# Kernel tuning notes

Measured on AMD Instinct MI355X. Metric: run time of the kernel, lower is better.

## Reference

```python
import jax, jax.numpy as jnp
import numpy as np

B, S, D, H = 8, 1300, 1080, 12
DK = D // H  # 90
FF = 3 * D   # 3240
EPS = 1e-5


def _layernorm(x, g, b):
    m = jnp.mean(x, axis=-1, keepdims=True)
    v = jnp.var(x, axis=-1, keepdims=True)
    return (x - m) * jax.lax.rsqrt(v + EPS) * g + b


def _rotate_half(x):
    x1, x2 = jnp.split(x, 2, axis=-1)
    return jnp.concatenate([-x2, x1], axis=-1)


def _rope(x, cos, sin):
    # x: [B,H,S,DK]; cos/sin: [S,DK] broadcast over batch/heads
    return x * cos + _rotate_half(x) * sin


def setup_inputs() -> dict:
    key = jax.random.key(0)
    ks = jax.random.split(key, 20)
    w = lambda k, sh: jax.random.normal(k, sh, dtype=jnp.float32) * 0.02
    inp = {
        'x': jax.random.normal(ks[0], (B, S, D), dtype=jnp.float32),
        'mask': jnp.tril(jnp.ones((S, S), dtype=jnp.int32))[None, None, :, :],
        'Wq': w(ks[1], (D, D)), 'bq': jnp.zeros((D,), jnp.float32),
        'Wk': w(ks[2], (D, D)), 'bk': jnp.zeros((D,), jnp.float32),
        'Wv': w(ks[3], (D, D)), 'bv': jnp.zeros((D,), jnp.float32),
        'Wo': w(ks[4], (D, D)), 'bo': jnp.zeros((D,), jnp.float32),
        'W1': w(ks[5], (D, FF)), 'b1': jnp.zeros((FF,), jnp.float32),
        'W2': w(ks[6], (FF, D)), 'b2': jnp.zeros((D,), jnp.float32),
        'W3': w(ks[7], (D, FF)), 'b3': jnp.zeros((FF,), jnp.float32),
        'ln1_g': jnp.ones((D,), jnp.float32), 'ln1_b': jnp.zeros((D,), jnp.float32),
        'ln2_g': jnp.ones((D,), jnp.float32), 'ln2_b': jnp.zeros((D,), jnp.float32),
    }
    # RoPE tables (buffers, not trainable)
    inv_freq = 1.0 / (10000.0 ** (jnp.arange(0, DK, 2, dtype=jnp.float32) / DK))
    t = jnp.arange(S, dtype=jnp.float32)
    freqs = t[:, None] * inv_freq[None, :]          # [S, DK/2]
    emb = jnp.concatenate([freqs, freqs], axis=-1)  # [S, DK]
    inp['rope_cos'] = jnp.cos(emb)
    inp['rope_sin'] = jnp.sin(emb)
    return inp


def reference(x, mask, Wq, bq, Wk, bk, Wv, bv, Wo, bo,
              W1, b1, W2, b2, W3, b3, ln1_g, ln1_b, ln2_g, ln2_b,
              rope_cos, rope_sin):
    # pre-norm attention block
    x2 = _layernorm(x, ln1_g, ln1_b)
    q = (x2 @ Wq + bq).reshape(B, S, H, DK).transpose(0, 2, 1, 3)  # [B,H,S,DK]
    k = (x2 @ Wk + bk).reshape(B, S, H, DK).transpose(0, 2, 1, 3)
    v = (x2 @ Wv + bv).reshape(B, S, H, DK).transpose(0, 2, 1, 3)
    q = _rope(q, rope_cos, rope_sin)
    k = _rope(k, rope_cos, rope_sin)
    scores = jnp.einsum('bhqd,bhkd->bhqk', q, k) / jnp.sqrt(jnp.float32(DK))
    scores = jnp.where(mask == 0, jnp.float32(-1e9), scores)
    p = jax.nn.softmax(scores, axis=-1)
    attn = jnp.einsum('bhqk,bhkd->bhqd', p, v)
    attn = attn.transpose(0, 2, 1, 3).reshape(B, S, D)
    x = x + (attn @ Wo + bo)
    # pre-norm SwiGLU FFN block
    x2 = _layernorm(x, ln2_g, ln2_b)
    h = jax.nn.silu(x2 @ W1 + b1) * (x2 @ W3 + b3)
    x = x + (h @ W2 + b2)
    return x
```

## Files before the change

### kernel.cpp

```cpp
#include <hip/hip_runtime.h>
#include <hip/hip_bf16.h>
#include <cstdint>
#include <cstddef>

#define B_  8
#define S_  1300
#define D_  1080
#define H_  12
#define DK_ 90
#define FF_ 3240
#define MROWS (B_*S_)
#define KP1 1088
#define KP2 3264
#define SP  1312
#define QKVN 3240
#define QSCALE 0.105409255338946f

typedef __hip_bfloat16 bf16;
typedef __bf16 bf16x8 __attribute__((ext_vector_type(8)));
typedef float  f32x4  __attribute__((ext_vector_type(4)));
typedef unsigned short u16x8 __attribute__((ext_vector_type(8)));
typedef unsigned int   u32x4 __attribute__((ext_vector_type(4)));

__device__ __forceinline__ void gload16(const void* g, void* l) {
    __builtin_amdgcn_global_load_lds((const __attribute__((address_space(1))) void*)g,
                                     (__attribute__((address_space(3))) void*)l, 16, 0, 0);
}
__device__ __forceinline__ unsigned short bf16bits(float f) {
    bf16 b = __float2bfloat16(f);
    return *(unsigned short*)&b;
}
__device__ __forceinline__ bf16x8 dsr(unsigned byteaddr) {
    union { u32x4 u; bf16x8 b; } c;
    asm volatile("ds_read_b128 %0, %1" : "=&v"(c.u) : "v"(byteaddr));
    return c.b;
}

#define BAR()   __builtin_amdgcn_s_barrier()
#define LGKM0() asm volatile("s_waitcnt lgkmcnt(0)" ::: "memory")
#define SCB()   __builtin_amdgcn_sched_barrier(0)

__global__ __launch_bounds__(256) void zero_pads(bf16* __restrict__ buf)
{
    const int idx = blockIdx.x * 256 + threadIdx.x;
    if (idx >= MROWS * (KP1 - D_)) return;
    const int row = idx >> 3, col = D_ + (idx & 7);
    buf[(size_t)row * KP1 + col] = __float2bfloat16(0.f);
}

__global__ __launch_bounds__(256) void bcat(const float* __restrict__ bq,
    const float* __restrict__ bk, const float* __restrict__ bv,
    float* __restrict__ bqkv)
{
    const int i = blockIdx.x * 256 + threadIdx.x;
    if (i >= QKVN) return;
    bqkv[i] = (i < D_) ? bq[i] : (i < 2 * D_) ? bk[i - D_] : bv[i - 2 * D_];
}

__global__ __launch_bounds__(256) void castT(const float* __restrict__ W,
    bf16* __restrict__ WT, int K, int N, int KP)
{
    __shared__ unsigned short t[32][33];
    const int tx = threadIdx.x & 31, ty = threadIdx.x >> 5;
    const int k0 = blockIdx.x * 32, n0 = blockIdx.y * 32;
    #pragma unroll
    for (int i = 0; i < 4; ++i) {
        const int k = k0 + ty + 8 * i;
        const int n = n0 + tx;
        float v = (k < K && n < N) ? W[(size_t)k * N + n] : 0.f;
        t[ty + 8 * i][tx] = bf16bits(v);
    }
    __syncthreads();
    #pragma unroll
    for (int i = 0; i < 4; ++i) {
        const int n = n0 + ty + 8 * i;
        const int kk = k0 + tx;
        if (n < N && kk < KP) *(unsigned short*)&WT[(size_t)n * KP + kk] = t[tx][ty + 8 * i];
    }
}

__global__ __launch_bounds__(256) void ln_kernel(const float* __restrict__ x,
    const float* __restrict__ g, const float* __restrict__ b,
    bf16* __restrict__ y)
{
    __shared__ float xs[D_];
    __shared__ float red[8];
    const int row = blockIdx.x;
    const int tid = threadIdx.x;
    const float* xr = x + (size_t)row * D_;

    float s = 0.f, sq = 0.f;
    for (int d = tid; d < D_; d += 256) {
        float v = xr[d];
        xs[d] = v;
        s += v; sq += v * v;
    }
    #pragma unroll
    for (int off = 32; off > 0; off >>= 1) {
        s  += __shfl_down(s,  off, 64);
        sq += __shfl_down(sq, off, 64);
    }
    const int wave = tid >> 6, lane = tid & 63;
    if (lane == 0) { red[wave] = s; red[4 + wave] = sq; }
    __syncthreads();
    if (tid == 0) {
        float ts = 0.f, tq = 0.f;
        #pragma unroll
        for (int w = 0; w < 4; ++w) { ts += red[w]; tq += red[4 + w]; }
        red[0] = ts; red[4] = tq;
    }
    __syncthreads();
    const float mean = red[0] * (1.0f / D_);
    const float var  = red[4] * (1.0f / D_) - mean * mean;
    const float rstd = rsqrtf(var + 1e-5f);
    bf16* yr = y + (size_t)row * KP1;
    for (int d = tid; d < D_; d += 256)
        yr[d] = __float2bfloat16((xs[d] - mean) * rstd * g[d] + b[d]);
}

template<int MODE>
__global__ __launch_bounds__(256, 3) void gemm_bf16(
    const bf16* __restrict__ A, const bf16* __restrict__ BT,
    const float* __restrict__ bias, const float* __restrict__ res,
    float* __restrict__ Cf, bf16* __restrict__ Cb,
    int M, int N, int KP, int LDC, int NP)
{
    __shared__ unsigned short lds[24576];

    const int tid = threadIdx.x;
    const int w = tid >> 6, l = tid & 63;
    const int lr = l & 15, kq = l >> 4;
    const int m0 = blockIdx.y * 128, n0 = blockIdx.x * 128;

    const int rs = w * 16 + (l >> 2);
    const int sx = ((l & 3) ^ ((l >> 3) & 3)) * 8;
    const int ar0 = min(m0 + rs,      M - 1);
    const int ar1 = min(m0 + rs + 64, M - 1);
    const int br0 = min(n0 + rs,      N - 1);
    const int br1 = min(n0 + rs + 64, N - 1);
    const bf16* pa0 = A  + (size_t)ar0 * KP + sx;
    const bf16* pa1 = A  + (size_t)ar1 * KP + sx;
    const bf16* pb0 = BT + (size_t)br0 * KP + sx;
    const bf16* pb1 = BT + (size_t)br1 * KP + sx;

    const int wm = (w >> 1) * 64, wn = (w & 1) * 64;

    const unsigned ldsb = (unsigned)(size_t)(const __attribute__((address_space(3))) void*)&lds[0];
    const unsigned co = (unsigned)((kq ^ ((lr >> 1) & 3)) << 4);
    unsigned aoffB[4], boffB[4];
    #pragma unroll
    for (int i = 0; i < 4; ++i) {
        aoffB[i] = ldsb + (unsigned)((wm + i * 16 + lr) * 64) + co;
        boffB[i] = ldsb + 24576u + (unsigned)((wn + i * 16 + lr) * 64) + co;
    }

    f32x4 acc[4][4] = {};
    const int nkt = KP >> 5;

#define STAGE(t, sl) do { \
    gload16(pa0 + (size_t)(t) * 32, &lds[(sl) * 4096 + w * 512]); \
    gload16(pa1 + (size_t)(t) * 32, &lds[(sl) * 4096 + 2048 + w * 512]); \
    gload16(pb0 + (size_t)(t) * 32, &lds[12288 + (sl) * 4096 + w * 512]); \
    gload16(pb1 + (size_t)(t) * 32, &lds[12288 + (sl) * 4096 + 2048 + w * 512]); \
} while (0)

    STAGE(0, 0);
    STAGE(1, 1);

    int sc_ = 0;
    int ss_ = 2;
    for (int t = 0; t < nkt; ++t) {
        if (t + 1 < nkt) { asm volatile("s_waitcnt vmcnt(4)" ::: "memory"); }
        else             { asm volatile("s_waitcnt vmcnt(0)" ::: "memory"); }
        BAR(); SCB();
        if (t + 2 < nkt) STAGE(t + 2, ss_);

        const unsigned sb = (unsigned)(sc_ * 8192);
        bf16x8 af[4], bv[4];
        #pragma unroll
        for (int i = 0; i < 4; ++i) af[i] = dsr(aoffB[i] + sb);
        #pragma unroll
        for (int j = 0; j < 4; ++j) bv[j] = dsr(boffB[j] + sb);
        LGKM0(); SCB();
        #pragma unroll
        for (int i = 0; i < 4; ++i)
            #pragma unroll
            for (int j = 0; j < 4; ++j)
                acc[i][j] = __builtin_amdgcn_mfma_f32_16x16x32_bf16(af[i], bv[j], acc[i][j], 0, 0, 0);
        SCB();

        sc_ = (sc_ == 2) ? 0 : sc_ + 1;
        ss_ = (ss_ == 2) ? 0 : ss_ + 1;
    }
#undef STAGE

    #pragma unroll
    for (int j = 0; j < 4; ++j) {
        const int n = n0 + wn + j * 16 + lr;
        if (n >= NP) continue;
        const bool real = (n < N);
        const float bn = real ? bias[n] : 0.f;
        #pragma unroll
        for (int i = 0; i < 4; ++i) {
            const int rowb = m0 + wm + i * 16 + kq * 4;
            #pragma unroll
            for (int r = 0; r < 4; ++r) {
                const int m = rowb + r;
                if (m < M) {
                    const size_t off = (size_t)m * LDC + n;
                    float val = acc[i][j][r] + bn;
                    if (MODE == 0) Cf[off] = val;
                    if (MODE == 1) Cf[off] = val + res[off];
                    if (MODE == 3) Cb[off] = real ? __float2bfloat16(val) : __float2bfloat16(0.f);
                    if (MODE == 2) {
                        if (real) {
                            const float prev = __bfloat162float(Cb[off]);
                            const float sig  = 1.0f / (1.0f + __expf(-prev));
                            Cb[off] = __float2bfloat16(prev * sig * val);
                        } else {
                            Cb[off] = __float2bfloat16(0.f);
                        }
                    }
                }
            }
        }
    }
}

__global__ __launch_bounds__(256) void rope_qk(const bf16* __restrict__ qkv,
    const float* __restrict__ cosb, const float* __restrict__ sinb,
    bf16* __restrict__ Qa, bf16* __restrict__ Ka)
{
    const int s = blockIdx.x;
    const int b = blockIdx.y;
    const int tid = threadIdx.x;

    if (s >= S_) {
        for (int idx = tid; idx < H_ * 96; idx += 256) {
            const int h = idx / 96, c = idx - (idx / 96) * 96;
            const size_t o = ((size_t)(b * H_ + h) * SP + s) * 96 + c;
            Qa[o] = __float2bfloat16(0.f);
            Ka[o] = __float2bfloat16(0.f);
        }
        return;
    }

    const bf16* row = qkv + (size_t)(b * S_ + s) * QKVN;

    for (int idx = tid; idx < H_ * 45; idx += 256) {
        const int h = idx / 45, d = idx - (idx / 45) * 45;
        const float c1 = cosb[s * DK_ + d],      s1 = sinb[s * DK_ + d];
        const float c2 = cosb[s * DK_ + d + 45], s2 = sinb[s * DK_ + d + 45];
        const size_t o = ((size_t)(b * H_ + h) * SP + s) * 96;
        const float q1 = __bfloat162float(row[h * DK_ + d]);
        const float q2 = __bfloat162float(row[h * DK_ + d + 45]);
        Qa[o + d]      = __float2bfloat16((q1 * c1 - q2 * s1) * QSCALE);
        Qa[o + d + 45] = __float2bfloat16((q2 * c2 + q1 * s2) * QSCALE);
        const float k1 = __bfloat162float(row[D_ + h * DK_ + d]);
        const float k2 = __bfloat162float(row[D_ + h * DK_ + d + 45]);
        Ka[o + d]      = __float2bfloat16(k1 * c1 - k2 * s1);
        Ka[o + d + 45] = __float2bfloat16(k2 * c2 + k1 * s2);
    }
    for (int idx = tid; idx < H_ * 6; idx += 256) {
        const int h = idx / 6, c = 90 + (idx - (idx / 6) * 6);
        const size_t o = ((size_t)(b * H_ + h) * SP + s) * 96 + c;
        Qa[o] = __float2bfloat16(0.f);
        Ka[o] = __float2bfloat16(0.f);
    }
}

__global__ __launch_bounds__(256) void vtrans(const bf16* __restrict__ qkv,
    bf16* __restrict__ Vt)
{
    __shared__ float T[96][33];
    const int k0 = blockIdx.x * 32;
    const int bh = blockIdx.y;
    const int b = bh / H_, h = bh % H_;
    const int tid = threadIdx.x;

    for (int idx = tid; idx < 32 * 90; idx += 256) {
        const int r = idx / 90, d = idx - (idx / 90) * 90;
        const int s = k0 + r;
        T[d][r] = (s < S_) ?
            __bfloat162float(qkv[(size_t)(b * S_ + s) * QKVN + 2 * D_ + h * DK_ + d]) : 0.f;
    }
    for (int idx = tid; idx < 32 * 6; idx += 256) {
        const int r = idx / 6, d = 90 + (idx - (idx / 6) * 6);
        T[d][r] = 0.f;
    }
    __syncthreads();
    for (int idx = tid; idx < 96 * 4; idx += 256) {
        const int d = idx >> 2, kk = (idx & 3) * 8;
        u16x8 v;
        #pragma unroll
        for (int i = 0; i < 8; ++i) v[i] = bf16bits(T[d][kk + i]);
        *(u16x8*)(Vt + ((size_t)bh * 96 + d) * SP + k0 + kk) = v;
    }
}

__global__ __launch_bounds__(256) void attn_mfma(const bf16* __restrict__ Qa,
    const bf16* __restrict__ Ka, const bf16* __restrict__ Vt,
    bf16* __restrict__ ab)
{
    __shared__ unsigned short Qs[64][104];
    __shared__ unsigned short Ks[32][104];
    __shared__ unsigned short Vs[96][40];
    __shared__ unsigned short Ps[4][16][40];

    const int tid = threadIdx.x;
    const int w = tid >> 6, l = tid & 63;
    const int lr = l & 15, kq = l >> 4;
    const int qblk = (int)gridDim.x - 1 - (int)blockIdx.x;
    const int q0 = qblk * 64;
    const int bh = blockIdx.y;
    const int b = bh / H_, h = bh % H_;

    const bf16* Qg = Qa + (size_t)bh * SP * 96;
    const bf16* Kg = Ka + (size_t)bh * SP * 96;
    const bf16* Vg = Vt + (size_t)bh * 96 * SP;

    for (int c = tid; c < 768; c += 256) {
        const int row = c / 12, cc = c - row * 12;
        const int rg = q0 + row;
        u16x8 v = (u16x8)0;
        if (rg < SP) v = *(const u16x8*)(Qg + (size_t)rg * 96 + cc * 8);
        *(u16x8*)&Qs[row][cc * 8] = v;
    }
    __syncthreads();

    bf16x8 Qf[3];
    #pragma unroll
    for (int kf = 0; kf < 3; ++kf)
        Qf[kf] = *(const bf16x8*)&Qs[w * 16 + lr][kf * 32 + kq * 8];

    const int qw0 = q0 + w * 16;
    const int myq = qw0 + lr;
    const int wlq = (qw0 < S_) ? min(qw0 + 15, S_ - 1) : -1;
    const int lastq = min(q0 + 63, S_ - 1);
    const int ntiles = lastq / 32 + 1;

    f32x4 Of[6] = {};
    float mrun = -1e30f, lrun = 0.f;

    for (int kt = 0; kt < ntiles; ++kt) {
        const int k0 = kt * 32;
        __syncthreads();
        for (int c = tid; c < 384; c += 256) {
            const int row = c / 12, cc = c - (c / 12) * 12;
            *(u16x8*)&Ks[row][cc * 8] = *(const u16x8*)(Kg + (size_t)(k0 + row) * 96 + cc * 8);
        }
        for (int c = tid; c < 384; c += 256) {
            const int d = c >> 2, kk = (c & 3) * 8;
            *(u16x8*)&Vs[d][kk] = *(const u16x8*)(Vg + (size_t)d * SP + k0 + kk);
        }
        __syncthreads();

        if (k0 > wlq) continue;

        f32x4 sg0 = {0.f, 0.f, 0.f, 0.f}, sg1 = {0.f, 0.f, 0.f, 0.f};
        #pragma unroll
        for (int kf = 0; kf < 3; ++kf) {
            bf16x8 k0f = *(const bf16x8*)&Ks[lr][kf * 32 + kq * 8];
            bf16x8 k1f = *(const bf16x8*)&Ks[16 + lr][kf * 32 + kq * 8];
            sg0 = __builtin_amdgcn_mfma_f32_16x16x32_bf16(k0f, Qf[kf], sg0, 0, 0, 0);
            sg1 = __builtin_amdgcn_mfma_f32_16x16x32_bf16(k1f, Qf[kf], sg1, 0, 0, 0);
        }

        float e[8];
        float msub = -1e30f;
        #pragma unroll
        for (int r = 0; r < 4; ++r) {
            const int ka = k0 + 4 * kq + r;
            const int kb = ka + 16;
            const float a = (ka <= myq && ka < S_) ? sg0[r] : -1e30f;
            const float c = (kb <= myq && kb < S_) ? sg1[r] : -1e30f;
            e[r] = a; e[4 + r] = c;
            msub = fmaxf(msub, fmaxf(a, c));
        }
        msub = fmaxf(msub, __shfl_xor(msub, 16, 64));
        msub = fmaxf(msub, __shfl_xor(msub, 32, 64));
        const float nm = fmaxf(mrun, msub);
        const float resc = __expf(mrun - nm);
        mrun = nm;
        float ls = 0.f;
        #pragma unroll
        for (int i = 0; i < 8; ++i) {
            const float ev = (e[i] > -1e29f) ? __expf(e[i] - nm) : 0.f;
            e[i] = ev; ls += ev;
        }
        ls += __shfl_xor(ls, 16, 64);
        ls += __shfl_xor(ls, 32, 64);
        lrun = lrun * resc + ls;

        ushort4 p0, p1;
        p0.x = bf16bits(e[0]); p0.y = bf16bits(e[1]); p0.z = bf16bits(e[2]); p0.w = bf16bits(e[3]);
        p1.x = bf16bits(e[4]); p1.y = bf16bits(e[5]); p1.z = bf16bits(e[6]); p1.w = bf16bits(e[7]);
        *(ushort4*)&Ps[w][lr][4 * kq]      = p0;
        *(ushort4*)&Ps[w][lr][16 + 4 * kq] = p1;

        float rf[4];
        #pragma unroll
        for (int r = 0; r < 4; ++r) rf[r] = __shfl(resc, 4 * kq + r, 16);
        #pragma unroll
        for (int c = 0; c < 6; ++c)
            #pragma unroll
            for (int r = 0; r < 4; ++r)
                Of[c][r] *= rf[r];

        bf16x8 Pf = *(const bf16x8*)&Ps[w][lr][kq * 8];
        #pragma unroll
        for (int c = 0; c < 6; ++c) {
            bf16x8 Vf = *(const bf16x8*)&Vs[16 * c + lr][kq * 8];
            Of[c] = __builtin_amdgcn_mfma_f32_16x16x32_bf16(Pf, Vf, Of[c], 0, 0, 0);
        }
    }

    const float invq = 1.0f / lrun;
    float inv[4];
    #pragma unroll
    for (int r = 0; r < 4; ++r) inv[r] = __shfl(invq, 4 * kq + r, 16);
    #pragma unroll
    for (int c = 0; c < 6; ++c) {
        const int dim = 16 * c + lr;
        if (dim >= DK_) continue;
        #pragma unroll
        for (int r = 0; r < 4; ++r) {
            const int qrow = qw0 + 4 * kq + r;
            if (qrow < S_)
                ab[(size_t)(b * S_ + qrow) * KP1 + h * DK_ + dim] =
                    __float2bfloat16(Of[c][r] * inv[r]);
        }
    }
}

extern "C" void kernel_launch(void* const* d_in, const int* in_sizes, int n_in,
                              void* d_out, int out_size, void* d_ws, size_t ws_size,
                              hipStream_t stream)
{
    const float* x    = (const float*)d_in[0];
    const float* Wq   = (const float*)d_in[2];
    const float* bq   = (const float*)d_in[3];
    const float* Wk   = (const float*)d_in[4];
    const float* bk   = (const float*)d_in[5];
    const float* Wv   = (const float*)d_in[6];
    const float* bv   = (const float*)d_in[7];
    const float* Wo   = (const float*)d_in[8];
    const float* bo   = (const float*)d_in[9];
    const float* W1   = (const float*)d_in[10];
    const float* b1   = (const float*)d_in[11];
    const float* W2   = (const float*)d_in[12];
    const float* b2   = (const float*)d_in[13];
    const float* W3   = (const float*)d_in[14];
    const float* b3   = (const float*)d_in[15];
    const float* ln1g = (const float*)d_in[16];
    const float* ln1b = (const float*)d_in[17];
    const float* ln2g = (const float*)d_in[18];
    const float* ln2b = (const float*)d_in[19];
    const float* rc   = (const float*)d_in[20];
    const float* rs   = (const float*)d_in[21];
    float* out = (float*)d_out;

    char* wsb = (char*)d_ws;
    size_t off = 0;
    auto nxt = [&](size_t bytes) -> char* {
        char* p = wsb + off; off += (bytes + 255) & ~(size_t)255; return p;
    };
    bf16*  x2   = (bf16*)nxt((size_t)MROWS * KP1 * 2);
    bf16*  qkv  = (bf16*)nxt((size_t)MROWS * KP2 * 2);
    float* x1f  = (float*)nxt((size_t)MROWS * D_ * 4);
    bf16*  ab   = (bf16*)nxt((size_t)MROWS * KP1 * 2);
    bf16*  WqkvT= (bf16*)nxt((size_t)QKVN * KP1 * 2);
    bf16*  WoT  = (bf16*)nxt((size_t)D_ * KP1 * 2);
    bf16*  W1T  = (bf16*)nxt((size_t)FF_ * KP1 * 2);
    bf16*  W3T  = (bf16*)nxt((size_t)FF_ * KP1 * 2);
    bf16*  W2T  = (bf16*)nxt((size_t)D_ * KP2 * 2);
    bf16*  Qa   = (bf16*)nxt((size_t)B_ * H_ * SP * 96 * 2);
    bf16*  Ka   = (bf16*)nxt((size_t)B_ * H_ * SP * 96 * 2);
    float* bqkv = (float*)nxt((size_t)QKVN * 4);
    bf16*  Vt   = (bf16*)x1f;
    float* x1   = x1f;
    bf16*  hb   = qkv;

    const dim3 blk(256);
    const dim3 gF(26, 82);
    const dim3 gD(9, 82);
    const int padN = MROWS * (KP1 - D_);

    zero_pads<<<(padN + 255) / 256, blk, 0, stream>>>(x2);
    zero_pads<<<(padN + 255) / 256, blk, 0, stream>>>(ab);
    bcat<<<(QKVN + 255) / 256, blk, 0, stream>>>(bq, bk, bv, bqkv);

    castT<<<dim3(34, 34),  blk, 0, stream>>>(Wq, WqkvT,                    D_, D_, KP1);
    castT<<<dim3(34, 34),  blk, 0, stream>>>(Wk, WqkvT + (size_t)D_ * KP1, D_, D_, KP1);
    castT<<<dim3(34, 34),  blk, 0, stream>>>(Wv, WqkvT + (size_t)2*D_*KP1, D_, D_, KP1);
    castT<<<dim3(34, 34),  blk, 0, stream>>>(Wo, WoT, D_, D_, KP1);
    castT<<<dim3(34, 102), blk, 0, stream>>>(W1, W1T, D_, FF_, KP1);
    castT<<<dim3(34, 102), blk, 0, stream>>>(W3, W3T, D_, FF_, KP1);
    castT<<<dim3(102, 34), blk, 0, stream>>>(W2, W2T, FF_, D_, KP2);

    ln_kernel<<<MROWS, blk, 0, stream>>>(x, ln1g, ln1b, x2);
    gemm_bf16<3><<<gF, blk, 0, stream>>>(x2, WqkvT, bqkv, nullptr, nullptr, qkv,
                                         MROWS, QKVN, KP1, QKVN, QKVN);
    rope_qk<<<dim3(SP, B_), blk, 0, stream>>>(qkv, rc, rs, Qa, Ka);
    vtrans<<<dim3(41, B_ * H_), blk, 0, stream>>>(qkv, Vt);
    attn_mfma<<<dim3(21, B_ * H_), blk, 0, stream>>>(Qa, Ka, Vt, ab);
    gemm_bf16<1><<<gD, blk, 0, stream>>>(ab, WoT, bo, x, x1, nullptr, MROWS, D_, KP1, D_, D_);
    ln_kernel<<<MROWS, blk, 0, stream>>>(x1, ln2g, ln2b, x2);
    gemm_bf16<3><<<gF, blk, 0, stream>>>(x2, W1T, b1, nullptr, nullptr, hb, MROWS, FF_, KP1, KP2, KP2);
    gemm_bf16<2><<<gF, blk, 0, stream>>>(x2, W3T, b3, nullptr, nullptr, hb, MROWS, FF_, KP1, KP2, KP2);
    gemm_bf16<1><<<gD, blk, 0, stream>>>(hb, W2T, b2, x1, out, nullptr, MROWS, D_, KP2, D_, D_);
}
```

Baseline: 1.107 ms.

## Double attention query tile to 128 rows with two fragments per wave

Each attention block now covers 128 query rows, and each wave handles 32 rows as two 16-row MFMA fragments. Every K/V tile loaded into shared memory is therefore reused across twice as many queries, which halves K/V traffic and the number of barrier rounds per query. Tiles that lie entirely below the causal diagonal skip the per-element mask, and the masked-exp guard is dropped. The cost is more registers (two sets of accumulators and softmax state), larger LDS use, fewer blocks, and coarser causal load imbalance.

```diff
diff --git a/kernel.cpp b/kernel.cpp
--- a/kernel.cpp
+++ b/kernel.cpp
@@ -302,16 +302,16 @@
     const bf16* __restrict__ Ka, const bf16* __restrict__ Vt,
     bf16* __restrict__ ab)
 {
-    __shared__ unsigned short Qs[64][104];
+    __shared__ unsigned short Qs[128][104];
     __shared__ unsigned short Ks[32][104];
     __shared__ unsigned short Vs[96][40];
-    __shared__ unsigned short Ps[4][16][40];
+    __shared__ unsigned short Ps[4][32][40];
 
     const int tid = threadIdx.x;
     const int w = tid >> 6, l = tid & 63;
     const int lr = l & 15, kq = l >> 4;
     const int qblk = (int)gridDim.x - 1 - (int)blockIdx.x;
-    const int q0 = qblk * 64;
+    const int q0 = qblk * 128;
     const int bh = blockIdx.y;
     const int b = bh / H_, h = bh % H_;
 
@@ -319,7 +319,7 @@
     const bf16* Kg = Ka + (size_t)bh * SP * 96;
     const bf16* Vg = Vt + (size_t)bh * 96 * SP;
 
-    for (int c = tid; c < 768; c += 256) {
+    for (int c = tid; c < 1536; c += 256) {
         const int row = c / 12, cc = c - row * 12;
         const int rg = q0 + row;
         u16x8 v = (u16x8)0;
@@ -328,19 +328,23 @@
     }
     __syncthreads();
 
-    bf16x8 Qf[3];
-    #pragma unroll
-    for (int kf = 0; kf < 3; ++kf)
-        Qf[kf] = *(const bf16x8*)&Qs[w * 16 + lr][kf * 32 + kq * 8];
-
-    const int qw0 = q0 + w * 16;
-    const int myq = qw0 + lr;
-    const int wlq = (qw0 < S_) ? min(qw0 + 15, S_ - 1) : -1;
-    const int lastq = min(q0 + 63, S_ - 1);
+    bf16x8 Qf[2][3];
+    #pragma unroll
+    for (int f = 0; f < 2; ++f)
+        #pragma unroll
+        for (int kf = 0; kf < 3; ++kf)
+            Qf[f][kf] = *(const bf16x8*)&Qs[w * 32 + f * 16 + lr][kf * 32 + kq * 8];
+
+    const int qw0 = q0 + w * 32;
+    const int myq0 = qw0 + lr;
+    const int myq1 = qw0 + 16 + lr;
+    const int wlq = (qw0 < S_) ? min(qw0 + 31, S_ - 1) : -1;
+    const int lastq = min(q0 + 127, S_ - 1);
     const int ntiles = lastq / 32 + 1;
 
-    f32x4 Of[6] = {};
-    float mrun = -1e30f, lrun = 0.f;
+    f32x4 Of[2][6] = {};
+    float mr0 = -1e30f, lr0_ = 0.f;
+    float mr1 = -1e30f, lr1_ = 0.f;
 
     for (int kt = 0; kt < ntiles; ++kt) {
         const int k0 = kt * 32;
@@ -357,78 +361,113 @@
 
         if (k0 > wlq) continue;
 
-        f32x4 sg0 = {0.f, 0.f, 0.f, 0.f}, sg1 = {0.f, 0.f, 0.f, 0.f};
+        f32x4 sg00 = {0,0,0,0}, sg01 = {0,0,0,0}, sg10 = {0,0,0,0}, sg11 = {0,0,0,0};
         #pragma unroll
         for (int kf = 0; kf < 3; ++kf) {
             bf16x8 k0f = *(const bf16x8*)&Ks[lr][kf * 32 + kq * 8];
             bf16x8 k1f = *(const bf16x8*)&Ks[16 + lr][kf * 32 + kq * 8];
-            sg0 = __builtin_amdgcn_mfma_f32_16x16x32_bf16(k0f, Qf[kf], sg0, 0, 0, 0);
-            sg1 = __builtin_amdgcn_mfma_f32_16x16x32_bf16(k1f, Qf[kf], sg1, 0, 0, 0);
-        }
-
-        float e[8];
-        float msub = -1e30f;
+            sg00 = __builtin_amdgcn_mfma_f32_16x16x32_bf16(k0f, Qf[0][kf], sg00, 0, 0, 0);
+            sg01 = __builtin_amdgcn_mfma_f32_16x16x32_bf16(k1f, Qf[0][kf], sg01, 0, 0, 0);
+            sg10 = __builtin_amdgcn_mfma_f32_16x16x32_bf16(k0f, Qf[1][kf], sg10, 0, 0, 0);
+            sg11 = __builtin_amdgcn_mfma_f32_16x16x32_bf16(k1f, Qf[1][kf], sg11, 0, 0, 0);
+        }
+
+        float e0[8], e1[8];
+        const bool full = (k0 + 31 <= qw0) && (k0 + 31 < S_);
+        if (full) {
+            #pragma unroll
+            for (int r = 0; r < 4; ++r) {
+                e0[r] = sg00[r]; e0[4 + r] = sg01[r];
+                e1[r] = sg10[r]; e1[4 + r] = sg11[r];
+            }
+        } else {
+            #pragma unroll
+            for (int r = 0; r < 4; ++r) {
+                const int ka = k0 + 4 * kq + r;
+                const int kb = ka + 16;
+                e0[r]     = (ka <= myq0 && ka < S_) ? sg00[r] : -1e30f;
+                e0[4 + r] = (kb <= myq0 && kb < S_) ? sg01[r] : -1e30f;
+                e1[r]     = (ka <= myq1 && ka < S_) ? sg10[r] : -1e30f;
+                e1[4 + r] = (kb <= myq1 && kb < S_) ? sg11[r] : -1e30f;
+            }
+        }
+
+        float m0s = e0[0], m1s = e1[0];
+        #pragma unroll
+        for (int i = 1; i < 8; ++i) { m0s = fmaxf(m0s, e0[i]); m1s = fmaxf(m1s, e1[i]); }
+        m0s = fmaxf(m0s, __shfl_xor(m0s, 16, 64));
+        m0s = fmaxf(m0s, __shfl_xor(m0s, 32, 64));
+        m1s = fmaxf(m1s, __shfl_xor(m1s, 16, 64));
+        m1s = fmaxf(m1s, __shfl_xor(m1s, 32, 64));
+        const float nm0 = fmaxf(mr0, m0s), nm1 = fmaxf(mr1, m1s);
+        const float rs0 = __expf(mr0 - nm0), rs1 = __expf(mr1 - nm1);
+        mr0 = nm0; mr1 = nm1;
+        float ls0 = 0.f, ls1 = 0.f;
+        #pragma unroll
+        for (int i = 0; i < 8; ++i) {
+            e0[i] = __expf(e0[i] - nm0); ls0 += e0[i];
+            e1[i] = __expf(e1[i] - nm1); ls1 += e1[i];
+        }
+        ls0 += __shfl_xor(ls0, 16, 64); ls0 += __shfl_xor(ls0, 32, 64);
+        ls1 += __shfl_xor(ls1, 16, 64); ls1 += __shfl_xor(ls1, 32, 64);
+        lr0_ = lr0_ * rs0 + ls0;
+        lr1_ = lr1_ * rs1 + ls1;
+
+        ushort4 p;
+        p.x = bf16bits(e0[0]); p.y = bf16bits(e0[1]); p.z = bf16bits(e0[2]); p.w = bf16bits(e0[3]);
+        *(ushort4*)&Ps[w][lr][4 * kq] = p;
+        p.x = bf16bits(e0[4]); p.y = bf16bits(e0[5]); p.z = bf16bits(e0[6]); p.w = bf16bits(e0[7]);
+        *(ushort4*)&Ps[w][lr][16 + 4 * kq] = p;
+        p.x = bf16bits(e1[0]); p.y = bf16bits(e1[1]); p.z = bf16bits(e1[2]); p.w = bf16bits(e1[3]);
+        *(ushort4*)&Ps[w][16 + lr][4 * kq] = p;
+        p.x = bf16bits(e1[4]); p.y = bf16bits(e1[5]); p.z = bf16bits(e1[6]); p.w = bf16bits(e1[7]);
+        *(ushort4*)&Ps[w][16 + lr][16 + 4 * kq] = p;
+
+        float rf0[4], rf1[4];
         #pragma unroll
         for (int r = 0; r < 4; ++r) {
-            const int ka = k0 + 4 * kq + r;
-            const int kb = ka + 16;
-            const float a = (ka <= myq && ka < S_) ? sg0[r] : -1e30f;
-            const float c = (kb <= myq && kb < S_) ? sg1[r] : -1e30f;
-            e[r] = a; e[4 + r] = c;
-            msub = fmaxf(msub, fmaxf(a, c));
-        }
-        msub = fmaxf(msub, __shfl_xor(msub, 16, 64));
-        msub = fmaxf(msub, __shfl_xor(msub, 32, 64));
-        const float nm = fmaxf(mrun, msub);
-        const float resc = __expf(mrun - nm);
-        mrun = nm;
-        float ls = 0.f;
-        #pragma unroll
-        for (int i = 0; i < 8; ++i) {
-            const float ev = (e[i] > -1e29f) ? __expf(e[i] - nm) : 0.f;
-            e[i] = ev; ls += ev;
-        }
-        ls += __shfl_xor(ls, 16, 64);
-        ls += __shfl_xor(ls, 32, 64);
-        lrun = lrun * resc + ls;
-
-        ushort4 p0, p1;
-        p0.x = bf16bits(e[0]); p0.y = bf16bits(e[1]); p0.z = bf16bits(e[2]); p0.w = bf16bits(e[3]);
-        p1.x = bf16bits(e[4]); p1.y = bf16bits(e[5]); p1.z = bf16bits(e[6]); p1.w = bf16bits(e[7]);
-        *(ushort4*)&Ps[w][lr][4 * kq]      = p0;
-        *(ushort4*)&Ps[w][lr][16 + 4 * kq] = p1;
-
-        float rf[4];
-        #pragma unroll
-        for (int r = 0; r < 4; ++r) rf[r] = __shfl(resc, 4 * kq + r, 16);
+            rf0[r] = __shfl(rs0, 4 * kq + r, 16);
+            rf1[r] = __shfl(rs1, 4 * kq + r, 16);
+        }
         #pragma unroll
         for (int c = 0; c < 6; ++c)
             #pragma unroll
-            for (int r = 0; r < 4; ++r)
-                Of[c][r] *= rf[r];
-
-        bf16x8 Pf = *(const bf16x8*)&Ps[w][lr][kq * 8];
+            for (int r = 0; r < 4; ++r) {
+                Of[0][c][r] *= rf0[r];
+                Of[1][c][r] *= rf1[r];
+            }
+
+        bf16x8 Pf0 = *(const bf16x8*)&Ps[w][lr][kq * 8];
+        bf16x8 Pf1 = *(const bf16x8*)&Ps[w][16 + lr][kq * 8];
         #pragma unroll
         for (int c = 0; c < 6; ++c) {
             bf16x8 Vf = *(const bf16x8*)&Vs[16 * c + lr][kq * 8];
-            Of[c] = __builtin_amdgcn_mfma_f32_16x16x32_bf16(Pf, Vf, Of[c], 0, 0, 0);
-        }
-    }
-
-    const float invq = 1.0f / lrun;
-    float inv[4];
-    #pragma unroll
-    for (int r = 0; r < 4; ++r) inv[r] = __shfl(invq, 4 * kq + r, 16);
+            Of[0][c] = __builtin_amdgcn_mfma_f32_16x16x32_bf16(Pf0, Vf, Of[0][c], 0, 0, 0);
+            Of[1][c] = __builtin_amdgcn_mfma_f32_16x16x32_bf16(Pf1, Vf, Of[1][c], 0, 0, 0);
+        }
+    }
+
+    const float iq0 = 1.0f / lr0_, iq1 = 1.0f / lr1_;
+    float inv0[4], inv1[4];
+    #pragma unroll
+    for (int r = 0; r < 4; ++r) {
+        inv0[r] = __shfl(iq0, 4 * kq + r, 16);
+        inv1[r] = __shfl(iq1, 4 * kq + r, 16);
+    }
     #pragma unroll
     for (int c = 0; c < 6; ++c) {
         const int dim = 16 * c + lr;
         if (dim >= DK_) continue;
         #pragma unroll
         for (int r = 0; r < 4; ++r) {
-            const int qrow = qw0 + 4 * kq + r;
-            if (qrow < S_)
-                ab[(size_t)(b * S_ + qrow) * KP1 + h * DK_ + dim] =
-                    __float2bfloat16(Of[c][r] * inv[r]);
+            const int q_a = qw0 + 4 * kq + r;
+            const int q_b = qw0 + 16 + 4 * kq + r;
+            if (q_a < S_)
+                ab[(size_t)(b * S_ + q_a) * KP1 + h * DK_ + dim] =
+                    __float2bfloat16(Of[0][c][r] * inv0[r]);
+            if (q_b < S_)
+                ab[(size_t)(b * S_ + q_b) * KP1 + h * DK_ + dim] =
+                    __float2bfloat16(Of[1][c][r] * inv1[r]);
         }
     }
 }
@@ -503,7 +542,7 @@
                                          MROWS, QKVN, KP1, QKVN, QKVN);
     rope_qk<<<dim3(SP, B_), blk, 0, stream>>>(qkv, rc, rs, Qa, Ka);
     vtrans<<<dim3(41, B_ * H_), blk, 0, stream>>>(qkv, Vt);
-    attn_mfma<<<dim3(21, B_ * H_), blk, 0, stream>>>(Qa, Ka, Vt, ab);
+    attn_mfma<<<dim3(11, B_ * H_), blk, 0, stream>>>(Qa, Ka, Vt, ab);
     gemm_bf16<1><<<gD, blk, 0, stream>>>(ab, WoT, bo, x, x1, nullptr, MROWS, D_, KP1, D_, D_);
     ln_kernel<<<MROWS, blk, 0, stream>>>(x1, ln2g, ln2b, x2);
     gemm_bf16<3><<<gF, blk, 0, stream>>>(x2, W1T, b1, nullptr, nullptr, hb, MROWS, FF_, KP1, KP2, KP2);
```

New measurement: 1.126 ms. Within noise of the previous version (+1.7%).
